# Kernel tuning notes

Measured on AMD Instinct MI355X. Metric: run time of the kernel, lower is better.

Reference implementation:

```python
import jax, jax.numpy as jnp
import numpy as np

WINDOWS = [7, 15, 31, 63, 127]
MAX_W = max(WINDOWS)
PAD = MAX_W // 2 + 1  # 64, matches K.spatial_2d_padding amount
HALF = MAX_W // 2     # 63


def _sat(a):
    """Integral image (summed-area table) of zero-padded input, per original layer."""
    ap = jnp.pad(a, ((0, 0), (PAD, PAD), (PAD, PAD), (0, 0)))
    return jnp.cumsum(jnp.cumsum(ap, axis=1), axis=2)


def _multi_window_means(a):
    """Box means for all window sizes. a: [B,H,W,C] -> [B,n_wins,H,W,C].
    Computes the count SAT once (original redundantly recomputes it per window;
    math is identical)."""
    B, H, W, C = a.shape
    ii = _sat(a)
    cnt_ii = _sat(jnp.ones_like(a[:1, ..., :1]))  # [1, H+2P, W+2P, 1]

    def box(ii_, h, w):
        top = HALF - h // 2
        left = HALF - w // 2
        bot, right = top + h, left + w
        return (ii_[:, top:top + H, left:left + W]
                + ii_[:, bot:bot + H, right:right + W]
                - ii_[:, top:top + H, right:right + W]
                - ii_[:, bot:bot + H, left:left + W])

    means = [box(ii, h, h) / box(cnt_ii, h, h) for h in WINDOWS]
    return jnp.stack(means, axis=1)  # [B, n_wins, H, W, C]


def setup_inputs() -> dict:
    key = jax.random.key(0)
    k1, _ = jax.random.split(key)
    B, H, W, C = 8, 1024, 1024, 1
    n_wins = len(WINDOWS)
    x = jax.random.uniform(k1, (B, H, W, C), dtype=jnp.float32)  # normalized image in (0,1)
    k = jnp.full((1, n_wins, 1, 1, 1), 0.2, dtype=jnp.float32)   # init_k
    R = jnp.full((1, n_wins, 1, 1, 1), 0.5, dtype=jnp.float32)   # init_R
    return {"x": x, "k": k, "R": R}


def reference(x, k, R):
    E_x = _multi_window_means(x)          # [B,5,H,W,C]
    E_x2 = _multi_window_means(x * x)
    dev_x = jnp.sqrt(jnp.maximum(E_x2 - E_x * E_x, 1e-6))
    T = E_x * (1.0 + k * (dev_x / R - 1.0))
    return T.astype(jnp.float32)
```

## Files before the change

kernel.cpp:

```cpp
#include <hip/hip_runtime.h>
#include <cstddef>

#define B_ 8
#define H_ 1024
#define W_ 1024
#define NW_ 5
#define CH_ 4
#define NCH_ (H_ / CH_)

__global__ __launch_bounds__(256) void k_rowpart(const float* __restrict__ x,
                                                 float* __restrict__ P1,
                                                 float* __restrict__ P2,
                                                 float* __restrict__ part1,
                                                 float* __restrict__ part2) {
  const int b = blockIdx.y;
  const int wave = threadIdx.x >> 6, lane = threadIdx.x & 63;
  const int y0 = blockIdx.x * 16 + wave * CH_;

  float4 acc1[4], acc2[4];
  #pragma unroll
  for (int c = 0; c < 4; ++c) {
    acc1[c] = make_float4(0.f, 0.f, 0.f, 0.f);
    acc2[c] = make_float4(0.f, 0.f, 0.f, 0.f);
  }

  #pragma unroll
  for (int rr = 0; rr < CH_; ++rr) {
    const int y = y0 + rr;
    const size_t rowoff = ((size_t)b * H_ + y) * W_;
    float carry1 = 0.f, carry2 = 0.f;
    #pragma unroll
    for (int c = 0; c < 4; ++c) {
      const float4 v = reinterpret_cast<const float4*>(x + rowoff + c * 256)[lane];
      float l1[4], l2[4];
      l1[0] = v.x - 0.5f;
      l1[1] = l1[0] + (v.y - 0.5f);
      l1[2] = l1[1] + (v.z - 0.5f);
      l1[3] = l1[2] + (v.w - 0.5f);
      l2[0] = v.x * v.x - (1.0f / 3.0f);
      l2[1] = l2[0] + (v.y * v.y - (1.0f / 3.0f));
      l2[2] = l2[1] + (v.z * v.z - (1.0f / 3.0f));
      l2[3] = l2[2] + (v.w * v.w - (1.0f / 3.0f));
      const float s1 = l1[3], s2 = l2[3];
      float inc1 = s1, inc2 = s2;
      #pragma unroll
      for (int off = 1; off < 64; off <<= 1) {
        const float t1 = __shfl_up(inc1, off);
        const float t2 = __shfl_up(inc2, off);
        if (lane >= off) { inc1 += t1; inc2 += t2; }
      }
      const float base1 = carry1 + inc1 - s1;
      const float base2 = carry2 + inc2 - s2;
      acc1[c].x += base1 + l1[0]; acc1[c].y += base1 + l1[1];
      acc1[c].z += base1 + l1[2]; acc1[c].w += base1 + l1[3];
      acc2[c].x += base2 + l2[0]; acc2[c].y += base2 + l2[1];
      acc2[c].z += base2 + l2[2]; acc2[c].w += base2 + l2[3];
      reinterpret_cast<float4*>(P1 + rowoff + c * 256)[lane] = acc1[c];
      reinterpret_cast<float4*>(P2 + rowoff + c * 256)[lane] = acc2[c];
      carry1 += __shfl(inc1, 63);
      carry2 += __shfl(inc2, 63);
    }
  }

  const int cc = y0 >> 2;
  const size_t po = ((size_t)(b * NCH_ + cc)) * W_;
  #pragma unroll
  for (int c = 0; c < 4; ++c) {
    reinterpret_cast<float4*>(part1 + po + c * 256)[lane] = acc1[c];
    reinterpret_cast<float4*>(part2 + po + c * 256)[lane] = acc2[c];
  }
}

__global__ __launch_bounds__(256) void k_ppscan(float* __restrict__ part1,
                                                float* __restrict__ part2) {
  const int xx = blockIdx.x * 256 + threadIdx.x;
  const int b = blockIdx.y;
  float r1 = 0.f, r2 = 0.f;
  #pragma unroll 8
  for (int c = 0; c < NCH_; ++c) {
    const size_t o = ((size_t)(b * NCH_ + c)) * W_ + xx;
    const float t1 = part1[o], t2 = part2[o];
    part1[o] = r1; part2[o] = r2;
    r1 += t1; r2 += t2;
  }
}

__global__ __launch_bounds__(256) void k_out(const float* __restrict__ S1,
                                             const float* __restrict__ S2,
                                             const float* __restrict__ pp1,
                                             const float* __restrict__ pp2,
                                             const float* __restrict__ kk,
                                             const float* __restrict__ RR,
                                             float* __restrict__ out) {
  const int i = blockIdx.x;
  const int xcd = i & 7;
  const int s = i >> 3;
  const int b = s >> 7;
  const int y = xcd * 128 + (s & 127);
  const int t = threadIdx.x;

  __shared__ float lds[2 * NW_ * W_];

  const float* base1 = S1 + (size_t)b * H_ * W_;
  const float* base2 = S2 + (size_t)b * H_ * W_;
  const float* pb1 = pp1 + (size_t)b * NCH_ * W_;
  const float* pb2 = pp2 + (size_t)b * NCH_ * W_;
  const int rad[NW_] = {3, 7, 15, 31, 63};

  #pragma unroll
  for (int w = 0; w < NW_; ++w) {
    const int r = rad[w];
    const int yB = min(y + r, H_ - 1);
    const int ccB = yB >> 2;
    float4 fb1 = reinterpret_cast<const float4*>(base1 + (size_t)yB * W_)[t];
    float4 fb2 = reinterpret_cast<const float4*>(base2 + (size_t)yB * W_)[t];
    const float4 qb1 = reinterpret_cast<const float4*>(pb1 + (size_t)ccB * W_)[t];
    const float4 qb2 = reinterpret_cast<const float4*>(pb2 + (size_t)ccB * W_)[t];
    fb1.x += qb1.x; fb1.y += qb1.y; fb1.z += qb1.z; fb1.w += qb1.w;
    fb2.x += qb2.x; fb2.y += qb2.y; fb2.z += qb2.z; fb2.w += qb2.w;
    float4 ft1 = {0.f, 0.f, 0.f, 0.f}, ft2 = {0.f, 0.f, 0.f, 0.f};
    const int yT = y - r - 1;
    if (yT >= 0) {
      const int ccT = yT >> 2;
      ft1 = reinterpret_cast<const float4*>(base1 + (size_t)yT * W_)[t];
      ft2 = reinterpret_cast<const float4*>(base2 + (size_t)yT * W_)[t];
      const float4 qt1 = reinterpret_cast<const float4*>(pb1 + (size_t)ccT * W_)[t];
      const float4 qt2 = reinterpret_cast<const float4*>(pb2 + (size_t)ccT * W_)[t];
      ft1.x += qt1.x; ft1.y += qt1.y; ft1.z += qt1.z; ft1.w += qt1.w;
      ft2.x += qt2.x; ft2.y += qt2.y; ft2.z += qt2.z; ft2.w += qt2.w;
    }
    float4 d1, d2;
    d1.x = fb1.x - ft1.x; d1.y = fb1.y - ft1.y; d1.z = fb1.z - ft1.z; d1.w = fb1.w - ft1.w;
    d2.x = fb2.x - ft2.x; d2.y = fb2.y - ft2.y; d2.z = fb2.z - ft2.z; d2.w = fb2.w - ft2.w;
    reinterpret_cast<float4*>(lds + (size_t)(2 * w) * W_)[t] = d1;
    reinterpret_cast<float4*>(lds + (size_t)(2 * w + 1) * W_)[t] = d2;
  }
  __syncthreads();

  #pragma unroll
  for (int w = 0; w < NW_; ++w) {
    const int r = rad[w];
    const float kw = kk[w];
    const float invR = __builtin_amdgcn_rcpf(RR[w]);
    const int yB = min(y + r, H_ - 1);
    const float rows = (float)(yB - max(y - r, 0) + 1);
    const float* D1 = lds + (size_t)(2 * w) * W_;
    const float* D2 = lds + (size_t)(2 * w + 1) * W_;
    float* orow = out + (((size_t)(b * NW_ + w)) * H_ + y) * W_;
    #pragma unroll
    for (int kp = 0; kp < 4; ++kp) {
      const int xx = t + kp * 256;
      const int xR = min(xx + r, W_ - 1);
      const int xL = xx - r - 1;
      float s1 = D1[xR];
      float s2 = D2[xR];
      if (xL >= 0) { s1 -= D1[xL]; s2 -= D2[xL]; }
      const float cols = (float)(xR - max(xx - r, 0) + 1);
      const float inv = __builtin_amdgcn_rcpf(rows * cols);
      const float Ex  = s1 * inv + 0.5f;
      const float Ex2 = s2 * inv + (1.0f / 3.0f);
      const float var = Ex2 - Ex * Ex;
      const float dev = __builtin_amdgcn_sqrtf(fmaxf(var, 1e-6f));
      orow[xx] = Ex * (1.0f + kw * (dev * invR - 1.0f));
    }
  }
}

extern "C" void kernel_launch(void* const* d_in, const int* in_sizes, int n_in,
                              void* d_out, int out_size, void* d_ws, size_t ws_size,
                              hipStream_t stream) {
  const float* x  = (const float*)d_in[0];
  const float* kk = (const float*)d_in[1];
  const float* RR = (const float*)d_in[2];
  float* out = (float*)d_out;

  const size_t plane = (size_t)B_ * H_ * W_;
  float* P1 = (float*)d_ws;
  float* P2 = P1 + plane;
  float* part1 = P2 + plane;
  float* part2 = part1 + (size_t)B_ * NCH_ * W_;

  k_rowpart <<<dim3(H_ / 16, B_),   256, 0, stream>>>(x, P1, P2, part1, part2);
  k_ppscan  <<<dim3(W_ / 256, B_),  256, 0, stream>>>(part1, part2);
  k_out     <<<dim3(B_ * H_),       256, 0, stream>>>(P1, P2, part1, part2, kk, RR, out);
}
```

Measured before the change: 269.6 us.

## Split serial chunk prefix scan into segmented scan plus fixup pass

Replaces the single-pass column scan over 256 chunk partials, which launched only 32 blocks, with a two-level scheme. Each of 16 segments is scanned independently, segment totals are written to a small super array, and a fixup kernel adds the preceding segment totals back in. This raises parallelism for the latency-bound middle stage, at the cost of an extra kernel launch and one more read-modify-write pass over the partials.

```diff
diff --git a/kernel.cpp b/kernel.cpp
--- a/kernel.cpp
+++ b/kernel.cpp
@@ -7,6 +7,8 @@
 #define NW_ 5
 #define CH_ 4
 #define NCH_ (H_ / CH_)
+#define SEG_ 16
+#define NSEG_ (NCH_ / SEG_)
 
 __global__ __launch_bounds__(256) void k_rowpart(const float* __restrict__ x,
                                                  float* __restrict__ P1,
@@ -71,17 +73,46 @@
   }
 }
 
-__global__ __launch_bounds__(256) void k_ppscan(float* __restrict__ part1,
-                                                float* __restrict__ part2) {
+__global__ __launch_bounds__(256) void k_segscan(float* __restrict__ part1,
+                                                 float* __restrict__ part2,
+                                                 float* __restrict__ super1,
+                                                 float* __restrict__ super2) {
   const int xx = blockIdx.x * 256 + threadIdx.x;
-  const int b = blockIdx.y;
+  const int seg = blockIdx.y, b = blockIdx.z;
+  const int cc0 = seg * SEG_;
   float r1 = 0.f, r2 = 0.f;
-  #pragma unroll 8
-  for (int c = 0; c < NCH_; ++c) {
-    const size_t o = ((size_t)(b * NCH_ + c)) * W_ + xx;
+  #pragma unroll
+  for (int i = 0; i < SEG_; ++i) {
+    const size_t o = ((size_t)(b * NCH_ + cc0 + i)) * W_ + xx;
     const float t1 = part1[o], t2 = part2[o];
     part1[o] = r1; part2[o] = r2;
     r1 += t1; r2 += t2;
+  }
+  const size_t so = ((size_t)(b * NSEG_ + seg)) * W_ + xx;
+  super1[so] = r1;
+  super2[so] = r2;
+}
+
+__global__ __launch_bounds__(256) void k_segfix(float* __restrict__ part1,
+                                                float* __restrict__ part2,
+                                                const float* __restrict__ super1,
+                                                const float* __restrict__ super2) {
+  const int seg = blockIdx.y;
+  if (seg == 0) return;
+  const int xx = blockIdx.x * 256 + threadIdx.x;
+  const int b = blockIdx.z;
+  float off1 = 0.f, off2 = 0.f;
+  for (int s = 0; s < seg; ++s) {
+    const size_t so = ((size_t)(b * NSEG_ + s)) * W_ + xx;
+    off1 += super1[so];
+    off2 += super2[so];
+  }
+  const int cc0 = seg * SEG_;
+  #pragma unroll
+  for (int i = 0; i < SEG_; ++i) {
+    const size_t o = ((size_t)(b * NCH_ + cc0 + i)) * W_ + xx;
+    part1[o] += off1;
+    part2[o] += off2;
   }
 }
 
@@ -179,8 +210,11 @@
   float* P2 = P1 + plane;
   float* part1 = P2 + plane;
   float* part2 = part1 + (size_t)B_ * NCH_ * W_;
-
-  k_rowpart <<<dim3(H_ / 16, B_),   256, 0, stream>>>(x, P1, P2, part1, part2);
-  k_ppscan  <<<dim3(W_ / 256, B_),  256, 0, stream>>>(part1, part2);
-  k_out     <<<dim3(B_ * H_),       256, 0, stream>>>(P1, P2, part1, part2, kk, RR, out);
-}
+  float* super1 = part2 + (size_t)B_ * NCH_ * W_;
+  float* super2 = super1 + (size_t)B_ * NSEG_ * W_;
+
+  k_rowpart <<<dim3(H_ / 16, B_),          256, 0, stream>>>(x, P1, P2, part1, part2);
+  k_segscan <<<dim3(W_/256, NSEG_, B_),    256, 0, stream>>>(part1, part2, super1, super2);
+  k_segfix  <<<dim3(W_/256, NSEG_, B_),    256, 0, stream>>>(part1, part2, super1, super2);
+  k_out     <<<dim3(B_ * H_),              256, 0, stream>>>(P1, P2, part1, part2, kk, RR, out);
+}
```

Measured after the change: 266.5 us. About the same (-1.2%).
